# Performance work log

Hardware: AMD Instinct MI355X
Metric: run time of the kernel (lower is better)

## Reference

```python
import jax, jax.numpy as jnp
import numpy as np

N = 100_000   # num nodes
E = 1_000_000 # num edges
F = 64        # feat_dim
H = 64        # hidden_dim
D = 64        # embed_dim


def _xavier(key, shape):
    limit = float(np.sqrt(6.0 / (shape[0] + shape[1])))
    return jax.random.uniform(key, shape, jnp.float32, -limit, limit)


def setup_inputs() -> dict:
    key = jax.random.key(0)
    ks = jax.random.split(key, 8)
    x = jax.random.normal(ks[0], (N, F), jnp.float32)
    edge_index = jax.random.randint(ks[1], (2, E), 0, N, dtype=jnp.int64)
    # GCNConv weights stored [in, out] (torch Linear transposed); biases zero-init
    return {
        "x": x,
        "edge_index": edge_index,
        "W1": _xavier(ks[2], (F, H)), "b1": jnp.zeros((H,), jnp.float32),
        "W2": _xavier(ks[3], (H, H)), "b2": jnp.zeros((H,), jnp.float32),
        "W3": _xavier(ks[4], (H, D)), "b3": jnp.zeros((D,), jnp.float32),
        "fw1": _xavier(ks[5], (D, H)), "fb1": jnp.zeros((H,), jnp.float32),
        "fw2": _xavier(ks[6], (H, D)), "fb2": jnp.zeros((D,), jnp.float32),
    }


def _gcn_conv(x, src, dst, dinv, W, b):
    # GCNConv: out = D^{-1/2} (A+I) D^{-1/2} (x W) + b
    h = x @ W                                   # [N, out]
    norm = dinv[src] * dinv[dst]                # [E]
    msg = h[src] * norm[:, None]                # gather + scale: [E, out]
    agg = jax.ops.segment_sum(msg, dst, num_segments=N)
    agg = agg + h * (dinv * dinv)[:, None]      # self-loop term
    return agg + b


def reference(x, edge_index, W1, b1, W2, b2, W3, b3, fw1, fb1, fw2, fb2):
    src, dst = edge_index[0], edge_index[1]
    # degree with self-loops (symmetric normalization)
    deg = jax.ops.segment_sum(jnp.ones((E,), x.dtype), dst, num_segments=N) + 1.0
    dinv = jax.lax.rsqrt(deg)
    # eval mode: dropout(p=0.5, training=False) is identity
    h = jax.nn.relu(_gcn_conv(x, src, dst, dinv, W1, b1))
    h = jax.nn.relu(_gcn_conv(h, src, dst, dinv, W2, b2))
    h = jax.nn.relu(_gcn_conv(h, src, dst, dinv, W3, b3))
    h = jax.nn.relu(h @ fw1 + fb1)
    return h @ fw2 + fb2                        # node embeddings [N, D]
```

## Files before the change

### kernel.cpp

```cpp
#include <hip/hip_runtime.h>
#include <cstdint>
#include <cstddef>


#define CDIV(a, b) (((a) + (b) - 1) / (b))

typedef __attribute__((ext_vector_type(8))) short bf16x8;
typedef __attribute__((ext_vector_type(4))) float f32x4;

static constexpr int BKT_SHIFT = 11;
static constexpr int BKT_NODES = 1 << BKT_SHIFT;
static constexpr int BKT_CAP = 24576;

__device__ __forceinline__ void split_bf(float a, short& hi, short& lo) {
  unsigned u = __float_as_uint(a);
  unsigned r = u + (0x7FFF + ((u >> 16) & 1));
  hi = (short)(r >> 16);
  float hirec = __uint_as_float(r & 0xFFFF0000u);
  float res = a - hirec;
  lo = (short)(__float_as_uint(res) >> 16);
}

__device__ __forceinline__ unsigned short f2bf_rne(float a) {
  unsigned u = __float_as_uint(a);
  u += 0x7FFF + ((u >> 16) & 1);
  return (unsigned short)(u >> 16);
}

__device__ __forceinline__ float4 bf4_to_f4(uint2 u) {
  float4 v;
  v.x = __uint_as_float(u.x << 16);
  v.y = __uint_as_float(u.x & 0xFFFF0000u);
  v.z = __uint_as_float(u.y << 16);
  v.w = __uint_as_float(u.y & 0xFFFF0000u);
  return v;
}

__device__ __forceinline__ void split8(float4 x, float4 y, bf16x8& h, bf16x8& l) {
  float av[8] = {x.x, x.y, x.z, x.w, y.x, y.y, y.z, y.w};
#pragma unroll
  for (int j = 0; j < 8; ++j) {
    short hi, lo;
    split_bf(av[j], hi, lo);
    h[j] = hi;
    l[j] = lo;
  }
}

__device__ __forceinline__ float4 nt_ld4(const float* p) {
  f32x4 v = __builtin_nontemporal_load(reinterpret_cast<const f32x4*>(p));
  float4 r;
  r.x = v[0]; r.y = v[1]; r.z = v[2]; r.w = v[3];
  return r;
}

__global__ void k_zero_i32(int* __restrict__ p, int n) {
  int i = blockIdx.x * blockDim.x + threadIdx.x;
  if (i < n) p[i] = 0;
}

__global__ __launch_bounds__(256)
void k_bucket(const int* __restrict__ ei, int* __restrict__ bcnt,
              int2* __restrict__ pairs, int E) {
  __shared__ int hist[64], rbase[64], roff[64];
  int t = threadIdx.x;
  int chunk = (E + gridDim.x - 1) / gridDim.x;
  int e0 = blockIdx.x * chunk;
  int e1 = min(e0 + chunk, E);
  if (t < 64) hist[t] = 0;
  __syncthreads();
  for (int e = e0 + t; e < e1; e += 256) {
    int d = __builtin_nontemporal_load(&ei[E + e]);
    atomicAdd(&hist[d >> BKT_SHIFT], 1);
  }
  __syncthreads();
  if (t < 64) {
    roff[t] = 0;
    rbase[t] = hist[t] ? atomicAdd(&bcnt[t], hist[t]) : 0;
  }
  __syncthreads();
  for (int e = e0 + t; e < e1; e += 256) {
    int d = __builtin_nontemporal_load(&ei[E + e]);
    int s = __builtin_nontemporal_load(&ei[e]);
    int b = d >> BKT_SHIFT;
    int r = atomicAdd(&roff[b], 1);
    int idx = rbase[b] + r;
    if (idx < BKT_CAP) pairs[(size_t)b * BKT_CAP + idx] = make_int2(s, d);
  }
}

__global__ __launch_bounds__(1024)
void k_build(const int2* __restrict__ pairs, const int* __restrict__ bcnt,
             int* __restrict__ row_ptr, float* __restrict__ dinv,
             int* __restrict__ srcs, int N, int E, int K) {
  __shared__ int cnt[2048];
  __shared__ int deg[2048];
  __shared__ int ebase_sh;
  int b = blockIdx.x;
  int t = threadIdx.x;
  int lo = b << BKT_SHIFT;
  int range = min(BKT_NODES, N - lo);
  int sz = min(bcnt[b], BKT_CAP);
  if (t == 0) {
    int s = 0;
    for (int i = 0; i < b; ++i) s += bcnt[i];
    ebase_sh = s;
  }
  cnt[t] = 0;
  cnt[t + 1024] = 0;
  __syncthreads();
  int ebase = ebase_sh;
  const int2* pb = pairs + (size_t)b * BKT_CAP;
  for (int i = t; i < sz; i += 1024) {
    atomicAdd(&cnt[pb[i].y - lo], 1);
  }
  __syncthreads();
  deg[t] = cnt[t];
  deg[t + 1024] = cnt[t + 1024];
  __syncthreads();
  int offset = 1;
  for (int d2 = 1024; d2 > 0; d2 >>= 1) {
    if (t < d2) {
      int ai = offset * (2 * t + 1) - 1;
      int bi = offset * (2 * t + 2) - 1;
      cnt[bi] += cnt[ai];
    }
    offset <<= 1;
    __syncthreads();
  }
  if (t == 0) cnt[2047] = 0;
  __syncthreads();
  for (int d2 = 1; d2 < 2048; d2 <<= 1) {
    offset >>= 1;
    if (t < d2) {
      int ai = offset * (2 * t + 1) - 1;
      int bi = offset * (2 * t + 2) - 1;
      int tmp = cnt[ai];
      cnt[ai] = cnt[bi];
      cnt[bi] += tmp;
    }
    __syncthreads();
  }
  for (int i = t; i < range; i += 1024) {
    row_ptr[lo + i] = ebase + cnt[i];
    dinv[lo + i] = rsqrtf((float)deg[i] + 1.0f);
  }
  if (b == K - 1 && t == 0) row_ptr[N] = E;
  __syncthreads();
  for (int i = t; i < sz; i += 1024) {
    int2 p = pb[i];
    int pos = ebase + atomicAdd(&cnt[p.y - lo], 1);
    srcs[pos] = p.x;
  }
}

__global__ void k_prep(const float* __restrict__ w0, const float* __restrict__ w1,
                       const float* __restrict__ w2, const float* __restrict__ w3,
                       const float* __restrict__ w4, bf16x8* __restrict__ packed) {
  const float* W;
  switch (blockIdx.x) {
    case 0: W = w0; break;
    case 1: W = w1; break;
    case 2: W = w2; break;
    case 3: W = w3; break;
    default: W = w4; break;
  }
  int tid = threadIdx.x;
  int lane = tid & 63;
  int q = (tid >> 6) & 1;
  int t = tid >> 7;
  int col = lane & 15, quad = lane >> 4;
  bf16x8 hi8, lo8;
#pragma unroll
  for (int j = 0; j < 8; ++j) {
    int k = q * 32 + quad * 8 + j;
    short hi, lo;
    split_bf(W[k * 64 + t * 16 + col], hi, lo);
    hi8[j] = hi;
    lo8[j] = lo;
  }
  size_t base = (size_t)blockIdx.x * 1024 + ((t * 2 + q) * 2) * 64 + lane;
  packed[base] = hi8;
  packed[base + 64] = lo8;
}

__global__ __launch_bounds__(256, 4)
void k_mm(const float* __restrict__ in, const bf16x8* __restrict__ Wp,
          const float* __restrict__ dinv, unsigned short* __restrict__ out, int n) {
  int lane = threadIdx.x & 63;
  int col = lane & 15, quad = lane >> 4;
  int tile = (blockIdx.x * blockDim.x + threadIdx.x) >> 6;
  int ntiles = (n + 15) >> 4;
  if (tile >= ntiles) return;

  bf16x8 wh[4][2], wl[4][2];
#pragma unroll
  for (int t = 0; t < 4; ++t)
#pragma unroll
    for (int q = 0; q < 2; ++q) {
      wh[t][q] = Wp[((t * 2 + q) * 2) * 64 + lane];
      wl[t][q] = Wp[((t * 2 + q) * 2 + 1) * 64 + lane];
    }

  int row0 = tile << 4;
  int ar = row0 + col;
  if (ar > n - 1) ar = n - 1;
  const float* arow = in + (size_t)ar * 64 + quad * 8;
  float4 a0 = nt_ld4(arow), a1 = nt_ld4(arow + 4);
  float4 a2 = nt_ld4(arow + 32), a3 = nt_ld4(arow + 36);

  bf16x8 ah[2], al[2];
  split8(a0, a1, ah[0], al[0]);
  split8(a2, a3, ah[1], al[1]);

  f32x4 acc[4];
#pragma unroll
  for (int t = 0; t < 4; ++t) acc[t] = (f32x4){0.f, 0.f, 0.f, 0.f};
#pragma unroll
  for (int t = 0; t < 4; ++t)
#pragma unroll
    for (int q = 0; q < 2; ++q) {
      acc[t] = __builtin_amdgcn_mfma_f32_16x16x32_bf16(ah[q], wh[t][q], acc[t], 0, 0, 0);
      acc[t] = __builtin_amdgcn_mfma_f32_16x16x32_bf16(ah[q], wl[t][q], acc[t], 0, 0, 0);
      acc[t] = __builtin_amdgcn_mfma_f32_16x16x32_bf16(al[q], wh[t][q], acc[t], 0, 0, 0);
    }
  float dv[4];
#pragma unroll
  for (int r = 0; r < 4; ++r) {
    int row = row0 + quad * 4 + r;
    dv[r] = (row < n) ? dinv[row] : 0.0f;
  }
#pragma unroll
  for (int t = 0; t < 4; ++t)
#pragma unroll
    for (int r = 0; r < 4; ++r) {
      int row = row0 + quad * 4 + r;
      if (row < n) out[(size_t)row * 64 + t * 16 + col] = f2bf_rne(acc[t][r] * dv[r]);
    }
}

template <bool HEAD>
__global__ __launch_bounds__(256, 4)
void k_agg_mm(const unsigned short* __restrict__ hws, const float* __restrict__ dinv,
              const int* __restrict__ row_ptr, const int* __restrict__ srcs,
              const float* __restrict__ bagg,
              const bf16x8* __restrict__ Wp1, const float* __restrict__ b1p,
              const bf16x8* __restrict__ Wp2, const float* __restrict__ b2p,
              void* __restrict__ out, int n) {
  constexpr int LDP = 68;
  __shared__ float a_sh[16 * LDP];
  int tid = threadIdx.x;
  int g = tid >> 4;
  int fg = tid & 15;
  int row0 = blockIdx.x << 4;
  const uint2* hw2 = (const uint2*)hws;

  int node = row0 + g;
  bool valid = node < n;
  int nd = valid ? node : (n - 1);
  uint2 su = hw2[(size_t)nd * 16 + fg];
  int p0 = 0, p1 = 0;
  if (valid) {
    p0 = row_ptr[node];
    p1 = row_ptr[node + 1];
  }
  float4 acc = make_float4(0.f, 0.f, 0.f, 0.f);
  for (int p = p0; p < p1; p += 4) {
    int i1 = (p + 1 < p1) ? p + 1 : p;
    int i2 = (p + 2 < p1) ? p + 2 : p;
    int i3 = (p + 3 < p1) ? p + 3 : p;
    int s0 = __builtin_nontemporal_load(&srcs[p]);
    int s1 = __builtin_nontemporal_load(&srcs[i1]);
    int s2 = __builtin_nontemporal_load(&srcs[i2]);
    int s3 = __builtin_nontemporal_load(&srcs[i3]);
    float4 v0 = bf4_to_f4(hw2[(size_t)s0 * 16 + fg]);
    float4 v1 = bf4_to_f4(hw2[(size_t)s1 * 16 + fg]);
    float4 v2 = bf4_to_f4(hw2[(size_t)s2 * 16 + fg]);
    float4 v3 = bf4_to_f4(hw2[(size_t)s3 * 16 + fg]);
    float m1 = (p + 1 < p1) ? 1.f : 0.f;
    float m2 = (p + 2 < p1) ? 1.f : 0.f;
    float m3 = (p + 3 < p1) ? 1.f : 0.f;
    acc.x += v0.x;
    acc.y += v0.y;
    acc.z += v0.z;
    acc.w += v0.w;
    acc.x = fmaf(m1, v1.x, acc.x);
    acc.y = fmaf(m1, v1.y, acc.y);
    acc.z = fmaf(m1, v1.z, acc.z);
    acc.w = fmaf(m1, v1.w, acc.w);
    acc.x = fmaf(m2, v2.x, acc.x);
    acc.y = fmaf(m2, v2.y, acc.y);
    acc.z = fmaf(m2, v2.z, acc.z);
    acc.w = fmaf(m2, v2.w, acc.w);
    acc.x = fmaf(m3, v3.x, acc.x);
    acc.y = fmaf(m3, v3.y, acc.y);
    acc.z = fmaf(m3, v3.z, acc.z);
    acc.w = fmaf(m3, v3.w, acc.w);
  }
  {
    float di = valid ? dinv[node] : 0.f;
    float4 selfv = bf4_to_f4(su);
    float4 b4 = ((const float4*)bagg)[fg];
    float4 r = make_float4(0.f, 0.f, 0.f, 0.f);
    if (valid) {
      r.x = fmaxf(fmaf(di, acc.x + selfv.x, b4.x), 0.f);
      r.y = fmaxf(fmaf(di, acc.y + selfv.y, b4.y), 0.f);
      r.z = fmaxf(fmaf(di, acc.z + selfv.z, b4.z), 0.f);
      r.w = fmaxf(fmaf(di, acc.w + selfv.w, b4.w), 0.f);
    }
    *(float4*)&a_sh[g * LDP + (fg << 2)] = r;
  }
  __syncthreads();

  int lane = threadIdx.x & 63;
  int wave = threadIdx.x >> 6;
  int col = lane & 15, quad = lane >> 4;
  const float* arow = &a_sh[col * LDP + (quad << 3)];
  float4 a0 = *(const float4*)(arow);
  float4 a1 = *(const float4*)(arow + 4);
  float4 a2 = *(const float4*)(arow + 32);
  float4 a3 = *(const float4*)(arow + 36);
  bf16x8 ah[2], al[2];
  split8(a0, a1, ah[0], al[0]);
  split8(a2, a3, ah[1], al[1]);

  bf16x8 wh[2], wl[2];
#pragma unroll
  for (int q = 0; q < 2; ++q) {
    wh[q] = Wp1[((wave * 2 + q) * 2) * 64 + lane];
    wl[q] = Wp1[((wave * 2 + q) * 2 + 1) * 64 + lane];
  }
  f32x4 acc1 = (f32x4){0.f, 0.f, 0.f, 0.f};
#pragma unroll
  for (int q = 0; q < 2; ++q) {
    acc1 = __builtin_amdgcn_mfma_f32_16x16x32_bf16(ah[q], wh[q], acc1, 0, 0, 0);
    acc1 = __builtin_amdgcn_mfma_f32_16x16x32_bf16(ah[q], wl[q], acc1, 0, 0, 0);
    acc1 = __builtin_amdgcn_mfma_f32_16x16x32_bf16(al[q], wh[q], acc1, 0, 0, 0);
  }

  if constexpr (!HEAD) {
#pragma unroll
    for (int r = 0; r < 4; ++r) {
      int row = row0 + (quad << 2) + r;
      if (row < n) {
        ((unsigned short*)out)[(size_t)row * 64 + wave * 16 + col] =
            f2bf_rne(acc1[r] * dinv[row]);
      }
    }
  } else {
    __shared__ float h_sh[16 * LDP];
    float bv1 = b1p[wave * 16 + col];
#pragma unroll
    for (int r = 0; r < 4; ++r) {
      h_sh[((quad << 2) + r) * LDP + wave * 16 + col] = fmaxf(acc1[r] + bv1, 0.f);
    }
    __syncthreads();
    const float* hrow = &h_sh[col * LDP + (quad << 3)];
    float4 h0 = *(const float4*)(hrow);
    float4 h1 = *(const float4*)(hrow + 4);
    float4 h2 = *(const float4*)(hrow + 32);
    float4 h3 = *(const float4*)(hrow + 36);
    bf16x8 ah2[2], al2[2];
    split8(h0, h1, ah2[0], al2[0]);
    split8(h2, h3, ah2[1], al2[1]);
    bf16x8 wh2[2], wl2[2];
#pragma unroll
    for (int q = 0; q < 2; ++q) {
      wh2[q] = Wp2[((wave * 2 + q) * 2) * 64 + lane];
      wl2[q] = Wp2[((wave * 2 + q) * 2 + 1) * 64 + lane];
    }
    f32x4 acc2 = (f32x4){0.f, 0.f, 0.f, 0.f};
#pragma unroll
    for (int q = 0; q < 2; ++q) {
      acc2 = __builtin_amdgcn_mfma_f32_16x16x32_bf16(ah2[q], wh2[q], acc2, 0, 0, 0);
      acc2 = __builtin_amdgcn_mfma_f32_16x16x32_bf16(ah2[q], wl2[q], acc2, 0, 0, 0);
      acc2 = __builtin_amdgcn_mfma_f32_16x16x32_bf16(al2[q], wh2[q], acc2, 0, 0, 0);
    }
    float bv2 = b2p[wave * 16 + col];
#pragma unroll
    for (int r = 0; r < 4; ++r) {
      int row = row0 + (quad << 2) + r;
      if (row < n) {
        ((float*)out)[(size_t)row * 64 + wave * 16 + col] = acc2[r] + bv2;
      }
    }
  }
}

extern "C" void kernel_launch(void* const* d_in, const int* in_sizes, int n_in,
                              void* d_out, int out_size, void* d_ws, size_t ws_size,
                              hipStream_t stream) {
  const float* x = (const float*)d_in[0];
  const int* ei = (const int*)d_in[1];
  const float* W1 = (const float*)d_in[2];
  const float* b1 = (const float*)d_in[3];
  const float* W2 = (const float*)d_in[4];
  const float* b2 = (const float*)d_in[5];
  const float* W3 = (const float*)d_in[6];
  const float* b3 = (const float*)d_in[7];
  const float* fw1 = (const float*)d_in[8];
  const float* fb1 = (const float*)d_in[9];
  const float* fw2 = (const float*)d_in[10];
  const float* fb2 = (const float*)d_in[11];
  float* out = (float*)d_out;

  const int N = in_sizes[0] / 64;
  const int E = in_sizes[1] / 2;
  const int K = CDIV(N, BKT_NODES);

  char* w = (char*)d_ws;
  auto take = [&](size_t bytes) -> char* {
    char* p = w;
    w += (bytes + 255) & ~(size_t)255;
    return p;
  };
  float* dinv = (float*)take((size_t)N * 4);
  int* row_ptr = (int*)take((size_t)(N + 1) * 4);
  int* bcnt = (int*)take((size_t)64 * 4);
  int* srcs = (int*)take((size_t)E * 4);
  bf16x8* wpack = (bf16x8*)take((size_t)5 * 1024 * 16);
  unsigned short* hwsA = (unsigned short*)take((size_t)N * 64 * 2);
  unsigned short* hwsB = (unsigned short*)take((size_t)N * 64 * 2);
  int2* pairs = (int2*)hwsA;

  const int B = 256;

  k_prep<<<5, 512, 0, stream>>>(W1, W2, W3, fw1, fw2, wpack);
  k_zero_i32<<<1, 64, 0, stream>>>(bcnt, 64);
  k_bucket<<<256, B, 0, stream>>>(ei, bcnt, pairs, E);
  k_build<<<K, 1024, 0, stream>>>(pairs, bcnt, row_ptr, dinv, srcs, N, E, K);

  const int ntiles = CDIV(N, 16);
  const int MMG = CDIV(ntiles, 4);

  k_mm<<<MMG, B, 0, stream>>>(x, wpack + 0 * 1024, dinv, hwsA, N);
  k_agg_mm<false><<<ntiles, B, 0, stream>>>(hwsA, dinv, row_ptr, srcs, b1,
                                            wpack + 1 * 1024, nullptr, nullptr, nullptr,
                                            hwsB, N);
  k_agg_mm<false><<<ntiles, B, 0, stream>>>(hwsB, dinv, row_ptr, srcs, b2,
                                            wpack + 2 * 1024, nullptr, nullptr, nullptr,
                                            hwsA, N);
  k_agg_mm<true><<<ntiles, B, 0, stream>>>(hwsA, dinv, row_ptr, srcs, b3,
                                           wpack + 3 * 1024, fb1, wpack + 4 * 1024, fb2,
                                           out, N);
}
```

Baseline: 263.8 us.

## Halve CSR build buckets and software-pipeline 8-wide neighbor gathers

```diff
diff --git a/kernel.cpp b/kernel.cpp
--- a/kernel.cpp
+++ b/kernel.cpp
@@ -8,9 +8,9 @@
 typedef __attribute__((ext_vector_type(8))) short bf16x8;
 typedef __attribute__((ext_vector_type(4))) float f32x4;
 
-static constexpr int BKT_SHIFT = 11;
+static constexpr int BKT_SHIFT = 10;
 static constexpr int BKT_NODES = 1 << BKT_SHIFT;
-static constexpr int BKT_CAP = 24576;
+static constexpr int BKT_CAP = 13312;
 
 __device__ __forceinline__ void split_bf(float a, short& hi, short& lo) {
   unsigned u = __float_as_uint(a);
@@ -62,19 +62,19 @@
 __global__ __launch_bounds__(256)
 void k_bucket(const int* __restrict__ ei, int* __restrict__ bcnt,
               int2* __restrict__ pairs, int E) {
-  __shared__ int hist[64], rbase[64], roff[64];
+  __shared__ int hist[128], rbase[128], roff[128];
   int t = threadIdx.x;
   int chunk = (E + gridDim.x - 1) / gridDim.x;
   int e0 = blockIdx.x * chunk;
   int e1 = min(e0 + chunk, E);
-  if (t < 64) hist[t] = 0;
+  if (t < 128) hist[t] = 0;
   __syncthreads();
   for (int e = e0 + t; e < e1; e += 256) {
     int d = __builtin_nontemporal_load(&ei[E + e]);
     atomicAdd(&hist[d >> BKT_SHIFT], 1);
   }
   __syncthreads();
-  if (t < 64) {
+  if (t < 128) {
     roff[t] = 0;
     rbase[t] = hist[t] ? atomicAdd(&bcnt[t], hist[t]) : 0;
   }
@@ -93,8 +93,8 @@
 void k_build(const int2* __restrict__ pairs, const int* __restrict__ bcnt,
              int* __restrict__ row_ptr, float* __restrict__ dinv,
              int* __restrict__ srcs, int N, int E, int K) {
-  __shared__ int cnt[2048];
-  __shared__ int deg[2048];
+  __shared__ int cnt[BKT_NODES];
+  __shared__ int deg[BKT_NODES];
   __shared__ int ebase_sh;
   int b = blockIdx.x;
   int t = threadIdx.x;
@@ -107,7 +107,6 @@
     ebase_sh = s;
   }
   cnt[t] = 0;
-  cnt[t + 1024] = 0;
   __syncthreads();
   int ebase = ebase_sh;
   const int2* pb = pairs + (size_t)b * BKT_CAP;
@@ -116,10 +115,9 @@
   }
   __syncthreads();
   deg[t] = cnt[t];
-  deg[t + 1024] = cnt[t + 1024];
   __syncthreads();
   int offset = 1;
-  for (int d2 = 1024; d2 > 0; d2 >>= 1) {
+  for (int d2 = BKT_NODES / 2; d2 > 0; d2 >>= 1) {
     if (t < d2) {
       int ai = offset * (2 * t + 1) - 1;
       int bi = offset * (2 * t + 2) - 1;
@@ -128,9 +126,9 @@
     offset <<= 1;
     __syncthreads();
   }
-  if (t == 0) cnt[2047] = 0;
-  __syncthreads();
-  for (int d2 = 1; d2 < 2048; d2 <<= 1) {
+  if (t == 0) cnt[BKT_NODES - 1] = 0;
+  __syncthreads();
+  for (int d2 = 1; d2 < BKT_NODES; d2 <<= 1) {
     offset >>= 1;
     if (t < d2) {
       int ai = offset * (2 * t + 1) - 1;
@@ -141,9 +139,9 @@
     }
     __syncthreads();
   }
-  for (int i = t; i < range; i += 1024) {
-    row_ptr[lo + i] = ebase + cnt[i];
-    dinv[lo + i] = rsqrtf((float)deg[i] + 1.0f);
+  if (t < range) {
+    row_ptr[lo + t] = ebase + cnt[t];
+    dinv[lo + t] = rsqrtf((float)deg[t] + 1.0f);
   }
   if (b == K - 1 && t == 0) row_ptr[N] = E;
   __syncthreads();
@@ -265,37 +263,42 @@
     p1 = row_ptr[node + 1];
   }
   float4 acc = make_float4(0.f, 0.f, 0.f, 0.f);
-  for (int p = p0; p < p1; p += 4) {
-    int i1 = (p + 1 < p1) ? p + 1 : p;
-    int i2 = (p + 2 < p1) ? p + 2 : p;
-    int i3 = (p + 3 < p1) ? p + 3 : p;
-    int s0 = __builtin_nontemporal_load(&srcs[p]);
-    int s1 = __builtin_nontemporal_load(&srcs[i1]);
-    int s2 = __builtin_nontemporal_load(&srcs[i2]);
-    int s3 = __builtin_nontemporal_load(&srcs[i3]);
-    float4 v0 = bf4_to_f4(hw2[(size_t)s0 * 16 + fg]);
-    float4 v1 = bf4_to_f4(hw2[(size_t)s1 * 16 + fg]);
-    float4 v2 = bf4_to_f4(hw2[(size_t)s2 * 16 + fg]);
-    float4 v3 = bf4_to_f4(hw2[(size_t)s3 * 16 + fg]);
-    float m1 = (p + 1 < p1) ? 1.f : 0.f;
-    float m2 = (p + 2 < p1) ? 1.f : 0.f;
-    float m3 = (p + 3 < p1) ? 1.f : 0.f;
-    acc.x += v0.x;
-    acc.y += v0.y;
-    acc.z += v0.z;
-    acc.w += v0.w;
-    acc.x = fmaf(m1, v1.x, acc.x);
-    acc.y = fmaf(m1, v1.y, acc.y);
-    acc.z = fmaf(m1, v1.z, acc.z);
-    acc.w = fmaf(m1, v1.w, acc.w);
-    acc.x = fmaf(m2, v2.x, acc.x);
-    acc.y = fmaf(m2, v2.y, acc.y);
-    acc.z = fmaf(m2, v2.z, acc.z);
-    acc.w = fmaf(m2, v2.w, acc.w);
-    acc.x = fmaf(m3, v3.x, acc.x);
-    acc.y = fmaf(m3, v3.y, acc.y);
-    acc.z = fmaf(m3, v3.z, acc.z);
-    acc.w = fmaf(m3, v3.w, acc.w);
+  if (p0 < p1) {
+    int s[8];
+#pragma unroll
+    for (int j = 0; j < 8; ++j) {
+      int ij = p0 + j;
+      ij = (ij < p1) ? ij : (p1 - 1);
+      s[j] = __builtin_nontemporal_load(&srcs[ij]);
+    }
+    for (int p = p0; p < p1; p += 8) {
+      uint2 u[8];
+#pragma unroll
+      for (int j = 0; j < 8; ++j) u[j] = hw2[(size_t)s[j] * 16 + fg];
+      int pn = p + 8;
+      if (pn < p1) {
+#pragma unroll
+        for (int j = 0; j < 8; ++j) {
+          int ij = pn + j;
+          ij = (ij < p1) ? ij : (p1 - 1);
+          s[j] = __builtin_nontemporal_load(&srcs[ij]);
+        }
+      }
+      float4 v0 = bf4_to_f4(u[0]);
+      acc.x += v0.x;
+      acc.y += v0.y;
+      acc.z += v0.z;
+      acc.w += v0.w;
+#pragma unroll
+      for (int j = 1; j < 8; ++j) {
+        float m = (p + j < p1) ? 1.f : 0.f;
+        float4 v = bf4_to_f4(u[j]);
+        acc.x = fmaf(m, v.x, acc.x);
+        acc.y = fmaf(m, v.y, acc.y);
+        acc.z = fmaf(m, v.z, acc.z);
+        acc.w = fmaf(m, v.w, acc.w);
+      }
+    }
   }
   {
     float di = valid ? dinv[node] : 0.f;
@@ -416,7 +419,7 @@
   };
   float* dinv = (float*)take((size_t)N * 4);
   int* row_ptr = (int*)take((size_t)(N + 1) * 4);
-  int* bcnt = (int*)take((size_t)64 * 4);
+  int* bcnt = (int*)take((size_t)128 * 4);
   int* srcs = (int*)take((size_t)E * 4);
   bf16x8* wpack = (bf16x8*)take((size_t)5 * 1024 * 16);
   unsigned short* hwsA = (unsigned short*)take((size_t)N * 64 * 2);
@@ -426,7 +429,7 @@
   const int B = 256;
 
   k_prep<<<5, 512, 0, stream>>>(W1, W2, W3, fw1, fw2, wpack);
-  k_zero_i32<<<1, 64, 0, stream>>>(bcnt, 64);
+  k_zero_i32<<<1, 128, 0, stream>>>(bcnt, 128);
   k_bucket<<<256, B, 0, stream>>>(ei, bcnt, pairs, E);
   k_build<<<K, 1024, 0, stream>>>(pairs, bcnt, row_ptr, dinv, srcs, N, E, K);
 
```

New measurement: 255.7 us. 1.03x faster.
